# Optimization experiments

Hardware: AMD Instinct MI355X
Metric: run time of the kernel (lower is better)

## Reference

```python
import jax, jax.numpy as jnp
import numpy as np

N_CLASSES = 80
N_BINS = 16
BOX_WEIGHT = 1.0
CLS_WEIGHT = 1.0
GAMMA = 2.0
ALPHA = 1.0


def setup_inputs() -> dict:
    key = jax.random.key(0)
    k0, k1, k2, kc, kxy, kwh, kl = jax.random.split(key, 7)
    B, N = 16, 50
    C = 4 * N_BINS + N_CLASSES  # 144
    feat0 = jax.random.normal(k0, (B, C, 80, 80), dtype=jnp.float32)
    feat1 = jax.random.normal(k1, (B, C, 40, 40), dtype=jnp.float32)
    feat2 = jax.random.normal(k2, (B, C, 20, 20), dtype=jnp.float32)
    cls = jax.random.randint(kc, (B, N, 1), 0, N_CLASSES).astype(jnp.float32)
    cxcy = jax.random.uniform(kxy, (B, N, 2), dtype=jnp.float32)
    wh = jax.random.uniform(kwh, (B, N, 2), dtype=jnp.float32) * 0.3
    layer = jax.random.randint(kl, (B, N, 1), 0, 3).astype(jnp.float32)
    targets = jnp.concatenate([cls, cxcy, wh, layer], axis=-1)  # [B,N,6]
    return {"feat0": feat0, "feat1": feat1, "feat2": feat2, "targets": targets}


def _layer_loss(feat, targets, layer_idx):
    # feat: [B, 4*N_BINS+N_CLASSES, H, W]; targets: [B, N, 6]
    B, C, H, W = feat.shape
    dist_pred = jnp.transpose(feat[:, : 4 * N_BINS], (0, 2, 3, 1)).reshape(B, H, W, 4, N_BINS)
    cls_pred = jnp.transpose(feat[:, 4 * N_BINS :], (0, 2, 3, 1))  # [B,H,W,nc]

    cls_t = targets[..., 0].astype(jnp.int32)            # [B,N]
    cx, cy = targets[..., 1], targets[..., 2]
    w, h = targets[..., 3], targets[..., 4]
    mask = (targets[..., 5].astype(jnp.int32) == layer_idx).astype(feat.dtype)  # [B,N]

    fx = jnp.clip((cx * W).astype(jnp.int32), 0, W - 1)  # [B,N]
    fy = jnp.clip((cy * H).astype(jnp.int32), 0, H - 1)
    bidx = jnp.arange(B)[:, None]

    # ---- focal classification loss (per positive target) ----
    logits = cls_pred[bidx, fy, fx]                      # [B,N,nc]
    logp = jax.nn.log_softmax(logits, axis=-1)
    ce = -jnp.take_along_axis(logp, cls_t[..., None], axis=-1)[..., 0]  # [B,N]
    pt = jnp.exp(-ce)
    focal = ALPHA * (1.0 - pt) ** GAMMA * ce
    cls_loss = jnp.sum(focal * mask)

    # ---- DFL box loss over 4 sides ----
    dist = dist_pred[bidx, fy, fx]                       # [B,N,4,n_bins]
    gt = jnp.stack([w / 2.0 * W, h / 2.0 * H, w / 2.0 * W, h / 2.0 * H], axis=-1)  # [B,N,4]
    tgt = jnp.clip(gt, 0.0, N_BINS - 1 - 1e-06)
    li = jnp.floor(tgt).astype(jnp.int32)
    wl = (li + 1).astype(feat.dtype) - tgt
    wr = tgt - li.astype(feat.dtype)
    lp = jax.nn.log_softmax(dist, axis=-1)               # [B,N,4,n_bins]
    lp_l = jnp.take_along_axis(lp, li[..., None], axis=-1)[..., 0]
    lp_r = jnp.take_along_axis(lp, jnp.minimum(li + 1, N_BINS - 1)[..., None], axis=-1)[..., 0]
    dfl = -(lp_l * wl + lp_r * wr)                       # [B,N,4]
    box_loss = jnp.sum(dfl.sum(-1) * mask)

    return cls_loss, box_loss


def reference(feat0, feat1, feat2, targets):
    total_cls = jnp.float32(0.0)
    total_box = jnp.float32(0.0)
    for layer_idx, feat in enumerate([feat0, feat1, feat2]):
        c, b = _layer_loss(feat, targets, layer_idx)
        total_cls = total_cls + c
        total_box = total_box + b
    total = CLS_WEIGHT * total_cls + BOX_WEIGHT * total_box
    return (total, total_cls, total_box)
```

## Files before the change

### kernel.cpp

```cpp
#include <hip/hip_runtime.h>
#include <math.h>

#define BATCH 16
#define NTGT  50
#define N_CLASSES 80
#define N_BINS 16

__global__ void __launch_bounds__(64) detloss_gather(
    const float* __restrict__ f0, const float* __restrict__ f1,
    const float* __restrict__ f2, const float* __restrict__ tgts,
    float2* __restrict__ partials) {
  const int t = blockIdx.x;
  const int b = t / NTGT;
  const int lane = threadIdx.x;

  const float* tp = tgts + (size_t)t * 6;
  const float t0 = tp[0], cx = tp[1], cy = tp[2], w = tp[3], h = tp[4], t5 = tp[5];
  const int cls_t = (int)t0;
  const int layer = (int)t5;

  const float* feat; int H, W;
  if (layer == 0)      { feat = f0; H = 80; W = 80; }
  else if (layer == 1) { feat = f1; H = 40; W = 40; }
  else                 { feat = f2; H = 20; W = 20; }

  int fx = (int)(cx * (float)W); fx = min(max(fx, 0), W - 1);
  int fy = (int)(cy * (float)H); fy = min(max(fy, 0), H - 1);

  const int C = 4 * N_BINS + N_CLASSES;
  const size_t hw = (size_t)H * (size_t)W;
  const float* base = feat + (size_t)b * C * hw + (size_t)fy * W + (size_t)fx;

  const float xd = base[(size_t)lane * hw];
  const float x1 = base[(size_t)(64 + lane) * hw];
  const float x2 = (lane < 16) ? base[(size_t)(128 + lane) * hw] : -INFINITY;

  float m = fmaxf(x1, x2);
  #pragma unroll
  for (int off = 32; off; off >>= 1) m = fmaxf(m, __shfl_xor(m, off));
  float s = expf(x1 - m) + ((lane < 16) ? expf(x2 - m) : 0.0f);
  #pragma unroll
  for (int off = 32; off; off >>= 1) s += __shfl_xor(s, off);
  const float lse = m + logf(s);
  const float v1 = __shfl(x1, cls_t & 63);
  const float v2 = __shfl(x2, cls_t & 15);
  const float logit_t = (cls_t < 64) ? v1 : v2;
  const float ce = lse - logit_t;
  const float pt = expf(-ce);
  const float om = 1.0f - pt;
  const float focal = om * om * ce;

  float m16 = xd;
  #pragma unroll
  for (int off = 8; off; off >>= 1) m16 = fmaxf(m16, __shfl_xor(m16, off));
  float s16 = expf(xd - m16);
  #pragma unroll
  for (int off = 8; off; off >>= 1) s16 += __shfl_xor(s16, off);
  const float lse16 = m16 + logf(s16);
  const float lp = xd - lse16;

  const int side = lane >> 4;
  const float gtv = (side & 1) ? (h * 0.5f * (float)H) : (w * 0.5f * (float)W);
  const float tv = fminf(fmaxf(gtv, 0.0f), (float)(N_BINS - 1) - 1e-6f);
  const int li = (int)tv;
  const float wl = (float)(li + 1) - tv;
  const float wr = tv - (float)li;
  const int gb = lane & 48;
  const float lp_l = __shfl(lp, gb | li);
  const float lp_r = __shfl(lp, gb | min(li + 1, N_BINS - 1));
  float dfl = -(lp_l * wl + lp_r * wr);
  dfl = ((lane & 15) == 0) ? dfl : 0.0f;
  float box = dfl;
  #pragma unroll
  for (int off = 32; off; off >>= 1) box += __shfl_xor(box, off);

  if (lane == 0) partials[t] = make_float2(focal, box);
}

__global__ void __launch_bounds__(256) detloss_reduce(
    const float2* __restrict__ partials, float* __restrict__ out) {
  __shared__ float sc[256], sb[256];
  const int tid = threadIdx.x;
  float c = 0.0f, bx = 0.0f;
  for (int i = tid; i < BATCH * NTGT; i += 256) {
    float2 p = partials[i]; c += p.x; bx += p.y;
  }
  sc[tid] = c; sb[tid] = bx;
  __syncthreads();
  #pragma unroll
  for (int off = 128; off; off >>= 1) {
    if (tid < off) { sc[tid] += sc[tid + off]; sb[tid] += sb[tid + off]; }
    __syncthreads();
  }
  if (tid == 0) {
    out[0] = sc[0] + sb[0];
    out[1] = sc[0];
    out[2] = sb[0];
  }
}

extern "C" void kernel_launch(void* const* d_in, const int* in_sizes, int n_in,
                              void* d_out, int out_size, void* d_ws, size_t ws_size,
                              hipStream_t stream) {
  const float* f0 = (const float*)d_in[0];
  const float* f1 = (const float*)d_in[1];
  const float* f2 = (const float*)d_in[2];
  const float* tg = (const float*)d_in[3];
  float2* partials = (float2*)d_ws;

  detloss_gather<<<BATCH * NTGT, 64, 0, stream>>>(f0, f1, f2, tg, partials);
  detloss_reduce<<<1, 256, 0, stream>>>(partials, (float*)d_out);
}
```

Measured before the change: 101.5 us.

## Fuse gather and reduce kernels via last-block atomic ticket

Merges the per-target gather kernel and the final reduction kernel into one launch, packing four targets per 256-thread block, and lets the last block to finish (detected with an atomic counter and thread fences) perform the final sum. Targets are loaded as float2 pairs. This removes a separate kernel launch and its dependency gap, but adds a hipMemsetAsync per call to reset the counter, which is itself an extra stream operation.

```diff
diff --git a/kernel.cpp b/kernel.cpp
--- a/kernel.cpp
+++ b/kernel.cpp
@@ -3,21 +3,30 @@
 
 #define BATCH 16
 #define NTGT  50
+#define NTOT  (BATCH * NTGT)
 #define N_CLASSES 80
 #define N_BINS 16
+#define NBLK  200
 
-__global__ void __launch_bounds__(64) detloss_gather(
+__global__ void __launch_bounds__(256) detloss_fused(
     const float* __restrict__ f0, const float* __restrict__ f1,
     const float* __restrict__ f2, const float* __restrict__ tgts,
-    float2* __restrict__ partials) {
-  const int t = blockIdx.x;
+    float2* __restrict__ partials, unsigned int* __restrict__ counter,
+    float* __restrict__ out) {
+  __shared__ float sc[256], sb[256];
+  __shared__ unsigned int s_ticket;
+
+  const int tid  = threadIdx.x;
+  const int wave = tid >> 6;
+  const int lane = tid & 63;
+  const int t = blockIdx.x * 4 + wave;
   const int b = t / NTGT;
-  const int lane = threadIdx.x;
 
-  const float* tp = tgts + (size_t)t * 6;
-  const float t0 = tp[0], cx = tp[1], cy = tp[2], w = tp[3], h = tp[4], t5 = tp[5];
-  const int cls_t = (int)t0;
-  const int layer = (int)t5;
+  const float2* tp2 = (const float2*)(tgts + (size_t)t * 6);
+  const float2 ta = tp2[0], tb = tp2[1], tc = tp2[2];
+  const float cx = ta.y, cy = tb.x, w = tb.y, h = tc.x;
+  const int cls_t = (int)ta.x;
+  const int layer = (int)tc.y;
 
   const float* feat; int H, W;
   if (layer == 0)      { feat = f0; H = 80; W = 80; }
@@ -75,27 +84,31 @@
   for (int off = 32; off; off >>= 1) box += __shfl_xor(box, off);
 
   if (lane == 0) partials[t] = make_float2(focal, box);
-}
 
-__global__ void __launch_bounds__(256) detloss_reduce(
-    const float2* __restrict__ partials, float* __restrict__ out) {
-  __shared__ float sc[256], sb[256];
-  const int tid = threadIdx.x;
-  float c = 0.0f, bx = 0.0f;
-  for (int i = tid; i < BATCH * NTGT; i += 256) {
-    float2 p = partials[i]; c += p.x; bx += p.y;
+  __syncthreads();
+  if (tid == 0) {
+    __threadfence();
+    s_ticket = atomicAdd(counter, 1u);
   }
-  sc[tid] = c; sb[tid] = bx;
   __syncthreads();
-  #pragma unroll
-  for (int off = 128; off; off >>= 1) {
-    if (tid < off) { sc[tid] += sc[tid + off]; sb[tid] += sb[tid + off]; }
+  if (s_ticket == NBLK - 1) {
+    __threadfence();
+    float c = 0.0f, bx = 0.0f;
+    for (int i = tid; i < NTOT; i += 256) {
+      float2 p = partials[i]; c += p.x; bx += p.y;
+    }
+    sc[tid] = c; sb[tid] = bx;
     __syncthreads();
-  }
-  if (tid == 0) {
-    out[0] = sc[0] + sb[0];
-    out[1] = sc[0];
-    out[2] = sb[0];
+    #pragma unroll
+    for (int off = 128; off; off >>= 1) {
+      if (tid < off) { sc[tid] += sc[tid + off]; sb[tid] += sb[tid + off]; }
+      __syncthreads();
+    }
+    if (tid == 0) {
+      out[0] = sc[0] + sb[0];
+      out[1] = sc[0];
+      out[2] = sb[0];
+    }
   }
 }
 
@@ -106,8 +119,12 @@
   const float* f1 = (const float*)d_in[1];
   const float* f2 = (const float*)d_in[2];
   const float* tg = (const float*)d_in[3];
+
   float2* partials = (float2*)d_ws;
+  unsigned int* counter = (unsigned int*)((char*)d_ws + 8192);
 
-  detloss_gather<<<BATCH * NTGT, 64, 0, stream>>>(f0, f1, f2, tg, partials);
-  detloss_reduce<<<1, 256, 0, stream>>>(partials, (float*)d_out);
+  hipMemsetAsync(counter, 0, sizeof(unsigned int), stream);
+
+  detloss_fused<<<NBLK, 256, 0, stream>>>(f0, f1, f2, tg, partials, counter,
+                                          (float*)d_out);
 }
```

Result: slower. 105.1 us (+3.5%).
